# Optimization experiments

Hardware: AMD Instinct MI355X
Metric: run time of the kernel (lower is better)

Reference implementation:

```python
import jax, jax.numpy as jnp
import numpy as np

B = 1024      # jets per batch
P = 150       # TOTAL_PARTICLES per jet
N = B * P     # total nodes
DEG = 16      # avg degree
E = N * DEG
H = 256       # GNN_HIDDEN_DIM
K = 6         # GNN_K
NC = 10       # NUM_CLUSTERS
IN = 3


def setup_inputs() -> dict:
    key = jax.random.key(0)
    ks = jax.random.split(key, 16)
    x = jax.random.normal(ks[0], (N, IN), jnp.float32)
    # kNN-like within-jet edges: each node sends to DEG random nodes of its own jet
    src = jnp.repeat(jnp.arange(N, dtype=jnp.int32), DEG)
    tgt = (src // P) * P + jax.random.randint(ks[1], (E,), 0, P, dtype=jnp.int32)
    edge_index = jnp.stack([src, tgt])  # [2, E]
    batch = jnp.arange(N, dtype=jnp.int32) // P  # sorted graph ids, exactly P per graph
    inp = dict(x=x, edge_index=edge_index, batch=batch)
    dims = [(IN, H), (H, H), (H, H), (H, H)]
    for i, (di, do) in enumerate(dims):
        s = 1.0 / np.sqrt(di)
        inp[f"W{i+1}"] = jax.random.uniform(ks[2 + i], (K, di, do), jnp.float32, -s, s)
        inp[f"b{i+1}"] = jnp.zeros((do,), jnp.float32)
    for i in range(3):
        inp[f"g{i+1}"] = jnp.ones((H,), jnp.float32)
        inp[f"be{i+1}"] = jnp.zeros((H,), jnp.float32)
    inp["centers"] = jax.random.normal(ks[10], (NC, 2), jnp.float32) * 0.2
    inp["log_temp"] = jnp.float32(2.0)
    return inp


def _lap_weights(src, tgt, n):
    # PyG ChebConv norm with lambda_max=2, sym normalization, self-loops removed:
    # scaled Laplacian L_hat = -D^{-1/2} A D^{-1/2} (zero diagonal)
    w = (src != tgt).astype(jnp.float32)          # remove self-loops
    deg = jax.ops.segment_sum(w, src, num_segments=n)
    dis = jnp.where(deg > 0, 1.0 / jnp.sqrt(deg), 0.0)
    return -(dis[src] * w * dis[tgt])             # [E]


def _cheb(x, W, b, src, tgt, lw, n):
    # Chebyshev recurrence: T0=x, T1=Lx, Tk=2L T_{k-1} - T_{k-2}
    prop = lambda h: jax.ops.segment_sum(lw[:, None] * h[src], tgt, num_segments=n)
    Tx0 = x
    out = Tx0 @ W[0]
    Tx1 = prop(Tx0)
    out = out + Tx1 @ W[1]
    for k in range(2, W.shape[0]):
        Tx2 = 2.0 * prop(Tx1) - Tx0
        out = out + Tx2 @ W[k]
        Tx0, Tx1 = Tx1, Tx2
    return out + b


def _bn(h, g, b):
    # BatchNorm1d, training-mode batch statistics (biased var), eps=1e-5
    m = h.mean(0)
    v = h.var(0)
    return (h - m) * jax.lax.rsqrt(v + 1e-5) * g + b


def reference(x, edge_index, batch, W1, b1, W2, b2, W3, b3, W4, b4,
              g1, be1, g2, be2, g3, be3, centers, log_temp):
    n = x.shape[0]
    src, tgt = edge_index[0], edge_index[1]
    lw = _lap_weights(src, tgt, n)
    lrelu = lambda h: jax.nn.leaky_relu(h, 0.01)
    h = lrelu(_bn(_cheb(x, W1, b1, src, tgt, lw, n), g1, be1))
    h = lrelu(_bn(_cheb(h, W2, b2, src, tgt, lw, n), g2, be2))
    h = lrelu(_bn(_cheb(h, W3, b3, src, tgt, lw, n), g3, be3))
    h = _cheb(h, W4, b4, src, tgt, lw, n)
    h = h / jnp.maximum(jnp.linalg.norm(h, axis=1, keepdims=True), 1e-12)  # F.normalize
    # to_dense_batch: batch is sorted with exactly P nodes per graph -> pure reshape,
    # node_mask is all True
    dense_h = h.reshape(B, P, -1)          # [B, P, H]
    dense_c = x[:, :2].reshape(B, P, 2)    # (eta, phi)
    dist = ((dense_c[:, :, None, :] - centers) ** 2).sum(-1)   # [B, P, NC]
    T = jnp.exp(jnp.clip(log_temp, -2.0, 3.0))
    assignment = jax.nn.softmax(-T * dist, axis=-1)            # mask is all-true
    pooled = jnp.einsum('bnk,bnd->bkd', assignment, dense_h)   # [B, NC, H]
    pooled = pooled / (assignment.sum(1)[:, :, None] + 1e-8)
    return pooled.reshape(B, -1)  # [B, NC*H]
```

## Files before the change

kernel.cpp:

```cpp
#include <hip/hip_runtime.h>
#include <cstdio>

#define NODES 153600
#define PJ 150
#define NJETS 1024
#define DEG 16
#define NEDGE (NODES*DEG)
#define HD 256
#define NCL 10

#define LSTR 192
#define TNS  64

typedef unsigned short u16;
typedef _Float16 f16;
typedef f16 f16x8 __attribute__((ext_vector_type(8)));
typedef u16 u16x8 __attribute__((ext_vector_type(8)));
typedef u16 u16x4 __attribute__((ext_vector_type(4)));
typedef float f32x4 __attribute__((ext_vector_type(4)));

__device__ inline float h2f(u16 u) { union { u16 s; f16 h; } v; v.s = u; return (float)v.h; }
__device__ inline u16 f2h(float f) { union { u16 s; f16 h; } v; v.h = (f16)f; return v.s; }
__device__ inline int swz(int seg, int key) { return (seg & ~7) | ((seg & 7) ^ (key & 7)); }

__global__ void k_diag(float* out, float code) {
  if (blockIdx.x == 0 && threadIdx.x == 0) out[0] = code;
}


__global__ __launch_bounds__(256) void k_discounts(const int* __restrict__ tgt,
                                                   int* __restrict__ counts,
                                                   float* __restrict__ dis) {
  int i = blockIdx.x*256 + threadIdx.x;
  if (i < NEDGE) atomicAdd(&counts[tgt[i]], 1);
  if (i < NODES) {
    int cnt = 0;
#pragma unroll
    for (int j = 0; j < DEG; ++j) cnt += (tgt[i*DEG + j] != i) ? 1 : 0;
    dis[i] = (cnt > 0) ? rsqrtf((float)cnt) : 0.f;
  }
}

__global__ __launch_bounds__(256) void k_scan(const int* __restrict__ counts, int* __restrict__ rowptr, int* __restrict__ cursor) {
  int j = blockIdx.x*256 + threadIdx.x;
  if (j >= NJETS) return;
  int run = j*PJ*DEG;
  for (int l = 0; l < PJ; ++l) {
    int idx = j*PJ + l;
    int cnt = counts[idx];
    rowptr[idx] = run;
    cursor[idx] = run;
    run += cnt;
  }
  if (j == 0) rowptr[NODES] = NEDGE;
}

__global__ __launch_bounds__(256) void k_fill(const int* __restrict__ src_, const int* __restrict__ tgt_,
                                              const float* __restrict__ dis, int* __restrict__ cursor,
                                              unsigned char* __restrict__ ccol, float* __restrict__ cw) {
  int e = blockIdx.x*256 + threadIdx.x;
  if (e >= NEDGE) return;
  int s = src_[e], t = tgt_[e];
  int pos = atomicAdd(&cursor[t], 1);
  ccol[pos] = (unsigned char)(s % PJ);
  cw[pos] = (s != t) ? -(dis[s]*dis[t]) : 0.f;
}

__global__ __launch_bounds__(256) void k_prepW(const float* __restrict__ Wa, const float* __restrict__ Wb,
                                               const float* __restrict__ Wc, u16* __restrict__ WT,
                                               float* __restrict__ stats ,
                                               float* __restrict__ rn) {
  int i = blockIdx.x*256 + threadIdx.x;
  if (i < 3*256*1536) {
    int layer = i / (256*1536);
    int rem = i - layer*(256*1536);
    int cout = rem / 1536, k = rem - cout*1536;
    int term = k >> 8, cin = k & 255;
    const float* W = (layer == 0) ? Wa : (layer == 1) ? Wb : Wc;
    WT[i] = f2h(W[(size_t)term*65536 + cin*256 + cout]);
  }
  if (i < 3*2*HD) stats[i] = 0.f;
  if (i < NODES) rn[i] = 0.f;
}

__global__ __launch_bounds__(512) void k_l1(const float* __restrict__ x,
                                            const int* __restrict__ rowptr,
                                            const unsigned char* __restrict__ ccol,
                                            const float* __restrict__ cw,
                                            const float* __restrict__ W1,
                                            const float* __restrict__ b1,
                                            float* __restrict__ stats,
                                            u16* __restrict__ outc) {
  __shared__ float Ta[450], Tb[450];
  __shared__ float Tall_s[PJ*18];
  __shared__ float wl[18*256];
  __shared__ float cw_s[PJ*DEG];
  __shared__ u16  col_s[PJ*DEG];
  __shared__ int  rp_s[PJ+1];
  int j = blockIdx.x, tid = threadIdx.x;
  int jb = j*PJ, e0 = jb*DEG;
  for (int i = tid; i < 18*256; i += 512) wl[i] = W1[i];
  for (int i = tid; i < PJ*DEG; i += 512) { cw_s[i] = cw[e0+i]; col_s[i] = (u16)ccol[e0+i]; }
  for (int i = tid; i < PJ+1; i += 512) rp_s[i] = rowptr[jb+i] - e0;
  if (tid < 450) Ta[tid] = x[(size_t)jb*3 + tid];
  __syncthreads();
  int r = tid/3, c = tid - r*3;
  float* cur = Ta; float* oth = Tb;
  if (tid < 450) Tall_s[r*18 + c] = cur[tid];
  for (int t = 1; t < 6; ++t) {
    if (tid < 450) {
      int es = rp_s[r], ee = rp_s[r+1];
      float acc = 0.f;
      for (int e = es; e < ee; ++e) acc += cw_s[e]*cur[(int)col_s[e]*3 + c];
      float v = (t == 1) ? acc : 2.f*acc - oth[tid];
      oth[tid] = v;
      Tall_s[r*18 + t*3 + c] = v;
    }
    __syncthreads();
    float* tmp = cur; cur = oth; oth = tmp;
  }
  int cc = tid & 255, rhalf = tid >> 8;
  float bc = b1[cc];
  float s = 0.f, s2 = 0.f;
  int r0 = rhalf*75;
  for (int rr = r0; rr < r0 + 75; ++rr) {
    float acc = 0.f;
#pragma unroll
    for (int i = 0; i < 18; ++i) acc += Tall_s[rr*18 + i] * wl[i*256 + cc];
    outc[(size_t)(jb+rr)*HD + cc] = f2h(acc);
    float vb = acc + bc;
    s += vb; s2 += vb*vb;
  }
  atomicAdd(&stats[cc], s);
  atomicAdd(&stats[HD + cc], s2);
}

template<int OMODE>
__global__ __launch_bounds__(1024, 4) void k_cheb(const u16* __restrict__ IN,
                                                  const u16* __restrict__ WTu,
                                                  const int* __restrict__ rowptr,
                                                  const unsigned char* __restrict__ ccol,
                                                  const float* __restrict__ cw,
                                                  const float* __restrict__ statsPrev,
                                                  const float* __restrict__ gP,
                                                  const float* __restrict__ beP,
                                                  const float* __restrict__ bP,
                                                  const float* __restrict__ bCur,
                                                  float* __restrict__ statsCur,
                                                  float* __restrict__ rn,
                                                  u16* __restrict__ OUTp) {
  __shared__ u16 Ls[160*LSTR];
  __shared__ u16 Tn[2][160*TNS];
  __shared__ u16 Tt[2][64*LSTR];
  __shared__ float bnA[HD], bnB[HD];
  int j = blockIdx.x, tid = threadIdx.x;
  int jb = j*PJ;
  int lane = tid & 63, wid = tid >> 6;
  int wm = wid >> 3, wn = wid & 7;
  int lr = lane & 15, lg = lane >> 4;
  int ph = wn >> 2, cs = wn & 3;
  int cown = cs*16 + lr;
  int key   = lr & 7;
  int segA0 = ((lg    ) ^ key) * 8;
  int segA1 = ((lg + 4) ^ key) * 8;
  int pOff[5] = { segA0, segA1, 64 + segA0, 64 + segA1, 128 + segA0 };
  int ep0 = ((cown >> 3) ^ ((lg & 1)*4 + 0)) * 8 + (cown & 7);
  int ep1 = ((cown >> 3) ^ ((lg & 1)*4 + 1)) * 8 + (cown & 7);
  int ep2 = ((cown >> 3) ^ ((lg & 1)*4 + 2)) * 8 + (cown & 7);
  int ep3 = ((cown >> 3) ^ ((lg & 1)*4 + 3)) * 8 + (cown & 7);
  int cownL = cown * LSTR;
  const f16* WT = (const f16*)WTu;
  const f16* wtb = WT + (size_t)(wn*32 + lr)*1536 + lg*8;

  if (tid < HD) {
    const float invN = 1.f/(float)NODES;
    float m = statsPrev[tid]*invN;
    float var = statsPrev[HD+tid]*invN - m*m;
    float A = rsqrtf(var + 1e-5f) * gP[tid];
    bnA[tid] = A;
    bnB[tid] = (bP[tid] - m)*A + beP[tid];
  }
  {
    u16x8 z = {0,0,0,0,0,0,0,0};
    for (int i = tid; i < 3840; i += 1024) *(u16x8*)&Ls[i*8] = z;
    for (int i = tid; i < 160; i += 1024) {
      int h = i >= 80 ? 1 : 0;
      int rem = i - h*80;
      int row = 150 + (rem >> 3), seg = rem & 7;
      *(u16x8*)&Tn[h][row*TNS + seg*8] = z;
    }
  }
  __syncthreads();
  if (tid < PJ) {
    int es = rowptr[jb + tid], ee = rowptr[jb + tid + 1];
    for (int e = es; e < ee; ++e) {
      int c = (int)ccol[e];
      int a = tid*LSTR + swz(c >> 3, tid)*8 + (c & 7);
      Ls[a] = f2h(h2f(Ls[a]) + 2.f*cw[e]);
    }
  }
  f32x4 acc[5][2];
#pragma unroll
  for (int a = 0; a < 5; ++a)
#pragma unroll
    for (int b = 0; b < 2; ++b) acc[a][b] = (f32x4)0.f;

  u16x4 tc0, tc1, tc2, tc3, tc4, tp0, tp1, tp2, tp3, tp4;

  for (int qp = 0; qp < 2; ++qp) {
    __syncthreads();
    for (int i = tid; i < 2400; i += 1024) {
      int h = (i >= 1200) ? 1 : 0;
      int rem = i - h*1200;
      int row = rem >> 3, seg = rem & 7;
      int c0 = (qp*2+h)*64 + seg*8;
      u16x8 v = *(const u16x8*)&IN[(size_t)(jb+row)*HD + c0];
      u16x8 o;
#pragma unroll
      for (int u = 0; u < 8; ++u) {
        float f = h2f(v[u])*bnA[c0+u] + bnB[c0+u];
        o[u] = f2h((f > 0.f) ? f : 0.01f*f);
      }
      *(u16x8*)&Tn[h][row*TNS + (seg ^ (row & 7))*8] = o;
    }
    __syncthreads();
    for (int i = tid; i < 2560; i += 1024) {
      int h = (i >= 1280) ? 1 : 0;
      int rem = i - h*1280;
      int c = rem & 63, m = rem >> 6;
      u16x8 v;
#pragma unroll
      for (int u = 0; u < 8; ++u) {
        int r = m*8 + u;
        v[u] = Tn[h][r*TNS + ((c >> 3) ^ (r & 7))*8 + (c & 7)];
      }
      *(u16x8*)&Tt[h][c*LSTR + swz(m, c)*8] = v;
    }
#define TINIT(MF, TC, TP) { int r0 = wm*80 + MF*16 + lg*4; u16x4 t; \
    t[0] = Tn[ph][(r0+0)*TNS + ep0]; t[1] = Tn[ph][(r0+1)*TNS + ep1]; \
    t[2] = Tn[ph][(r0+2)*TNS + ep2]; t[3] = Tn[ph][(r0+3)*TNS + ep3]; \
    TC = t; TP = t; }
    TINIT(0, tc0, tp0) TINIT(1, tc1, tp1) TINIT(2, tc2, tp2) TINIT(3, tc3, tp3) TINIT(4, tc4, tp4)
#undef TINIT
    __syncthreads();
#pragma unroll 1
    for (int t = 0; t < 6; ++t) {
#pragma unroll
      for (int h = 0; h < 2; ++h) {
        int kbase = t*256 + (qp*2+h)*64;
#pragma unroll
        for (int ks = 0; ks < 64; ks += 32) {
          int segA = (ks == 0) ? segA0 : segA1;
          f16x8 a[5], bv[2];
#pragma unroll
          for (int nf = 0; nf < 2; ++nf)
            bv[nf] = *(const f16x8*)&wtb[nf*24576 + kbase + ks];
#pragma unroll
          for (int mf = 0; mf < 5; ++mf) {
            int row = wm*80 + mf*16 + lr;
            a[mf] = *(const f16x8*)&Tn[h][row*TNS + segA];
          }
#pragma unroll
          for (int nf = 0; nf < 2; ++nf)
#pragma unroll
            for (int mf = 0; mf < 5; ++mf)
              acc[mf][nf] = __builtin_amdgcn_mfma_f32_16x16x32_f16(a[mf], bv[nf], acc[mf][nf], 0, 0, 0);
        }
      }
      if (t < 5) {
        f32x4 pacc[5];
#pragma unroll
        for (int mf = 0; mf < 5; ++mf) pacc[mf] = (f32x4)0.f;
#pragma unroll
        for (int ks = 0; ks < 5; ++ks) {
          f16x8 b = *(const f16x8*)&Tt[ph][cownL + pOff[ks]];
#pragma unroll
          for (int mf = 0; mf < 5; ++mf) {
            int row = wm*80 + mf*16 + lr;
            f16x8 a = *(const f16x8*)&Ls[row*LSTR + pOff[ks]];
            pacc[mf] = __builtin_amdgcn_mfma_f32_16x16x32_f16(a, b, pacc[mf], 0, 0, 0);
          }
        }
        __syncthreads();
#define TEPI(MF, TC, TP) { int r0 = wm*80 + MF*16 + lg*4; u16x4 o; \
        { float v0_ = (t == 0) ? 0.5f*pacc[MF][0] : pacc[MF][0] - h2f(TP[0]); o[0] = f2h(v0_); } \
        { float v1_ = (t == 0) ? 0.5f*pacc[MF][1] : pacc[MF][1] - h2f(TP[1]); o[1] = f2h(v1_); } \
        { float v2_ = (t == 0) ? 0.5f*pacc[MF][2] : pacc[MF][2] - h2f(TP[2]); o[2] = f2h(v2_); } \
        { float v3_ = (t == 0) ? 0.5f*pacc[MF][3] : pacc[MF][3] - h2f(TP[3]); o[3] = f2h(v3_); } \
        Tn[ph][(r0+0)*TNS + ep0] = o[0]; Tn[ph][(r0+1)*TNS + ep1] = o[1]; \
        Tn[ph][(r0+2)*TNS + ep2] = o[2]; Tn[ph][(r0+3)*TNS + ep3] = o[3]; \
        int sgT = wm*10 + MF*2 + (lg >> 1); \
        int segT = (sgT & ~7) | ((sgT & 7) ^ key); \
        *(u16x4*)&Tt[ph][cownL + segT*8 + (lg & 1)*4] = o; \
        TP = TC; TC = o; }
        TEPI(0, tc0, tp0) TEPI(1, tc1, tp1) TEPI(2, tc2, tp2) TEPI(3, tc3, tp3) TEPI(4, tc4, tp4)
#undef TEPI
        __syncthreads();
      }
    }
  }
  if (OMODE == 0) {
#pragma unroll
    for (int nf = 0; nf < 2; ++nf) {
      int col = wn*32 + nf*16 + lr;
      float bc = bCur[col];
      float s = 0.f, s2 = 0.f;
#pragma unroll
      for (int mf = 0; mf < 5; ++mf) {
        int row = wm*80 + mf*16 + lg*4;
#pragma unroll
        for (int e = 0; e < 4; ++e) {
          int r = row + e;
          if (r < PJ) {
            float v = acc[mf][nf][e];
            OUTp[(size_t)(jb+r)*HD + col] = f2h(v);
            float vb = v + bc;
            s += vb; s2 += vb*vb;
          }
        }
      }
      s  += __shfl_xor(s, 16, 64);  s  += __shfl_xor(s, 32, 64);
      s2 += __shfl_xor(s2, 16, 64); s2 += __shfl_xor(s2, 32, 64);
      if (lg == 0) {
        atomicAdd(&statsCur[col], s);
        atomicAdd(&statsCur[HD + col], s2);
      }
    }
  } else {
    float bc[2];
#pragma unroll
    for (int nf = 0; nf < 2; ++nf) bc[nf] = bCur[wn*32 + nf*16 + lr];
#pragma unroll
    for (int mf = 0; mf < 5; ++mf) {
      int row = wm*80 + mf*16 + lg*4;
#pragma unroll
      for (int e = 0; e < 4; ++e) {
        int r = row + e;
        float srow = 0.f;
        if (r < PJ) {
#pragma unroll
          for (int nf = 0; nf < 2; ++nf) {
            int col = wn*32 + nf*16 + lr;
            float v = acc[mf][nf][e];
            OUTp[(size_t)(jb+r)*HD + col] = f2h(v);
            float vb = v + bc[nf];
            srow += vb*vb;
          }
        }
        srow += __shfl_xor(srow, 1, 64);
        srow += __shfl_xor(srow, 2, 64);
        srow += __shfl_xor(srow, 4, 64);
        srow += __shfl_xor(srow, 8, 64);
        if (lr == 0 && r < PJ) atomicAdd(&rn[jb + r], srow);
      }
    }
  }
}


__global__ __launch_bounds__(256) void k_pool(const u16* __restrict__ h, const float* __restrict__ rn,
                                              const float* __restrict__ bias, const float* __restrict__ x,
                                              const float* __restrict__ centers, const float* __restrict__ log_temp,
                                              float* __restrict__ out) {
  __shared__ float a_s[PJ][NCL];
  __shared__ float colsum[NCL];
  __shared__ float inv_s[PJ];
  int j = blockIdx.x;
  int tid = threadIdx.x;
  float T = expf(fminf(fmaxf(log_temp[0], -2.f), 3.f));
  if (tid < PJ) {
    int g = j*PJ + tid;
    inv_s[tid] = 1.f / fmaxf(sqrtf(rn[g]), 1e-12f);
    float eta = x[(size_t)g*3], phi = x[(size_t)g*3 + 1];
    float d[NCL];
    float dmin = 1e30f;
#pragma unroll
    for (int k = 0; k < NCL; ++k) {
      float dx = eta - centers[2*k], dy = phi - centers[2*k+1];
      d[k] = dx*dx + dy*dy;
      dmin = fminf(dmin, d[k]);
    }
    float s = 0.f, ek[NCL];
#pragma unroll
    for (int k = 0; k < NCL; ++k) { ek[k] = expf(-T*(d[k]-dmin)); s += ek[k]; }
    float invs = 1.f/s;
#pragma unroll
    for (int k = 0; k < NCL; ++k) a_s[tid][k] = ek[k]*invs;
  }
  __syncthreads();
  if (tid < NCL) {
    float s = 0.f;
    for (int n = 0; n < PJ; ++n) s += a_s[n][tid];
    colsum[tid] = s;
  }
  __syncthreads();
  int c = tid;
  float bc = bias[c];
  float acc[NCL] = {};
  for (int n = 0; n < PJ; ++n) {
    float hv = (h2f(h[(size_t)(j*PJ + n)*HD + c]) + bc) * inv_s[n];
#pragma unroll
    for (int k = 0; k < NCL; ++k) acc[k] += a_s[n][k]*hv;
  }
#pragma unroll
  for (int k = 0; k < NCL; ++k)
    out[(size_t)j*(NCL*HD) + k*HD + c] = acc[k] / (colsum[k] + 1e-8f);
}


extern "C" void kernel_launch(void* const* d_in, const int* in_sizes, int n_in,
                              void* d_out, int out_size, void* d_ws, size_t ws_size,
                              hipStream_t stream) {
  (void)in_sizes; (void)n_in; (void)out_size;
  const float* x   = (const float*)d_in[0];
  const int*   ei  = (const int*)d_in[1];
  const int*   srcA = ei;
  const int*   tgtA = ei + NEDGE;
  const float* W1  = (const float*)d_in[3];
  const float* b1  = (const float*)d_in[4];
  const float* W2  = (const float*)d_in[5];
  const float* b2  = (const float*)d_in[6];
  const float* W3  = (const float*)d_in[7];
  const float* b3  = (const float*)d_in[8];
  const float* W4  = (const float*)d_in[9];
  const float* b4  = (const float*)d_in[10];
  const float* g1  = (const float*)d_in[11];
  const float* be1 = (const float*)d_in[12];
  const float* g2  = (const float*)d_in[13];
  const float* be2 = (const float*)d_in[14];
  const float* g3  = (const float*)d_in[15];
  const float* be3 = (const float*)d_in[16];
  const float* centers  = (const float*)d_in[17];
  const float* log_temp = (const float*)d_in[18];
  float* out = (float*)d_out;

  auto rb = [](size_t b) { return (b + 255) & ~(size_t)255; };
  size_t need = 2*rb((size_t)NODES*HD*2)
              + rb((size_t)3*256*1536*2)
              + 3*rb((size_t)NODES*4)
              + rb((size_t)(NODES+1)*4)
              + rb((size_t)NEDGE)
              + rb((size_t)NEDGE*4)
              + rb((size_t)3*2*HD*4)
              + rb((size_t)NODES*4);
  fprintf(stderr, "[kernel_launch] ws_size=%zu need=%zu\n", ws_size, need);
  if (d_ws == nullptr || ws_size < need) {
    float code = 1.0e6f + (float)(ws_size >> 20);
    k_diag<<<1, 1, 0, stream>>>(out, code);
    return;
  }

  char* wp = (char*)d_ws;
  auto alloc = [&](size_t b) -> void* {
    void* p = (void*)wp;
    wp += (b + 255) & ~(size_t)255;
    return p;
  };
  u16*   OUTA = (u16*)alloc((size_t)NODES*HD*2);
  u16*   OUTB = (u16*)alloc((size_t)NODES*HD*2);
  u16*   Wcat = (u16*)alloc((size_t)3*256*1536*2);
  float* dis  = (float*)alloc((size_t)NODES*4);
  int*   counts = (int*)alloc((size_t)NODES*4);
  int*   cursor = (int*)alloc((size_t)NODES*4);
  int*   rowptr = (int*)alloc((size_t)(NODES+1)*4);
  unsigned char* ccol = (unsigned char*)alloc((size_t)NEDGE);
  float* cw     = (float*)alloc((size_t)NEDGE*4);
  float* stats  = (float*)alloc((size_t)3*2*HD*4);
  float* rn     = (float*)alloc((size_t)NODES*4);
  float* s0 = stats, *s1 = stats + 512, *s2 = stats + 1024;

  hipMemsetAsync(counts, 0, (size_t)NODES*4, stream);
  k_discounts<<<(NEDGE+255)/256, 256, 0, stream>>>(tgtA, counts, dis);
  k_scan<<<(NJETS+255)/256, 256, 0, stream>>>(counts, rowptr, cursor);
  k_fill<<<(NEDGE+255)/256, 256, 0, stream>>>(srcA, tgtA, dis, cursor, ccol, cw);

  k_prepW<<<(3*256*1536+255)/256, 256, 0, stream>>>(W2, W3, W4, Wcat, stats, rn);

  k_l1<<<NJETS, 512, 0, stream>>>(x, rowptr, ccol, cw, W1, b1, s0, OUTA);

  k_cheb<0><<<NJETS, 1024, 0, stream>>>(OUTA, Wcat,            rowptr, ccol, cw, s0, g1, be1, b1, b2, s1, rn, OUTB);
  k_cheb<0><<<NJETS, 1024, 0, stream>>>(OUTB, Wcat + 393216,   rowptr, ccol, cw, s1, g2, be2, b2, b3, s2, rn, OUTA);
  k_cheb<1><<<NJETS, 1024, 0, stream>>>(OUTA, Wcat + 2*393216, rowptr, ccol, cw, s2, g3, be3, b3, b4, s2, rn, OUTB);

  k_pool<<<NJETS, 256, 0, stream>>>(OUTB, rn, b4, x, centers, log_temp, out);
}
```

Before: 1.273 ms.

## Stage Chebyshev output through shared memory for coalesced stores and hoist weight loads

Merges the separate shared buffers into one pool so the output tile can be staged in shared memory after the GEMM. The global write then becomes 16-byte coalesced row stores instead of scattered 2-byte per-lane writes. The weight fragments for each recurrence step are also all loaded up front, so global weight reads are issued together ahead of the MFMAs. This costs two extra block barriers, a shared-memory round trip, and more live registers.

```diff
diff --git a/kernel.cpp b/kernel.cpp
--- a/kernel.cpp
+++ b/kernel.cpp
@@ -11,6 +11,7 @@
 
 #define LSTR 192
 #define TNS  64
+#define OSTR 264
 
 typedef unsigned short u16;
 typedef _Float16 f16;
@@ -149,10 +150,13 @@
                                                   float* __restrict__ statsCur,
                                                   float* __restrict__ rn,
                                                   u16* __restrict__ OUTp) {
-  __shared__ u16 Ls[160*LSTR];
-  __shared__ u16 Tn[2][160*TNS];
-  __shared__ u16 Tt[2][64*LSTR];
+  __shared__ u16 SM[75776];
   __shared__ float bnA[HD], bnB[HD];
+  u16* Ls  = SM;
+  u16* Tn0 = SM + 30720;
+  u16* Tn1 = SM + 40960;
+  u16* Tt0 = SM + 51200;
+  u16* Tt1 = SM + 63488;
   int j = blockIdx.x, tid = threadIdx.x;
   int jb = j*PJ;
   int lane = tid & 63, wid = tid >> 6;
@@ -160,6 +164,8 @@
   int lr = lane & 15, lg = lane >> 4;
   int ph = wn >> 2, cs = wn & 3;
   int cown = cs*16 + lr;
+  u16* Tnp = ph ? Tn1 : Tn0;
+  u16* Ttp = ph ? Tt1 : Tt0;
   int key   = lr & 7;
   int segA0 = ((lg    ) ^ key) * 8;
   int segA1 = ((lg + 4) ^ key) * 8;
@@ -187,7 +193,8 @@
       int h = i >= 80 ? 1 : 0;
       int rem = i - h*80;
       int row = 150 + (rem >> 3), seg = rem & 7;
-      *(u16x8*)&Tn[h][row*TNS + seg*8] = z;
+      u16* TnH = h ? Tn1 : Tn0;
+      *(u16x8*)&TnH[row*TNS + seg*8] = z;
     }
   }
   __syncthreads();
@@ -221,59 +228,61 @@
         float f = h2f(v[u])*bnA[c0+u] + bnB[c0+u];
         o[u] = f2h((f > 0.f) ? f : 0.01f*f);
       }
-      *(u16x8*)&Tn[h][row*TNS + (seg ^ (row & 7))*8] = o;
+      u16* TnH = h ? Tn1 : Tn0;
+      *(u16x8*)&TnH[row*TNS + (seg ^ (row & 7))*8] = o;
     }
     __syncthreads();
     for (int i = tid; i < 2560; i += 1024) {
       int h = (i >= 1280) ? 1 : 0;
       int rem = i - h*1280;
       int c = rem & 63, m = rem >> 6;
+      u16* TnH = h ? Tn1 : Tn0;
+      u16* TtH = h ? Tt1 : Tt0;
       u16x8 v;
 #pragma unroll
       for (int u = 0; u < 8; ++u) {
         int r = m*8 + u;
-        v[u] = Tn[h][r*TNS + ((c >> 3) ^ (r & 7))*8 + (c & 7)];
+        v[u] = TnH[r*TNS + ((c >> 3) ^ (r & 7))*8 + (c & 7)];
       }
-      *(u16x8*)&Tt[h][c*LSTR + swz(m, c)*8] = v;
+      *(u16x8*)&TtH[c*LSTR + swz(m, c)*8] = v;
     }
 #define TINIT(MF, TC, TP) { int r0 = wm*80 + MF*16 + lg*4; u16x4 t; \
-    t[0] = Tn[ph][(r0+0)*TNS + ep0]; t[1] = Tn[ph][(r0+1)*TNS + ep1]; \
-    t[2] = Tn[ph][(r0+2)*TNS + ep2]; t[3] = Tn[ph][(r0+3)*TNS + ep3]; \
+    t[0] = Tnp[(r0+0)*TNS + ep0]; t[1] = Tnp[(r0+1)*TNS + ep1]; \
+    t[2] = Tnp[(r0+2)*TNS + ep2]; t[3] = Tnp[(r0+3)*TNS + ep3]; \
     TC = t; TP = t; }
     TINIT(0, tc0, tp0) TINIT(1, tc1, tp1) TINIT(2, tc2, tp2) TINIT(3, tc3, tp3) TINIT(4, tc4, tp4)
 #undef TINIT
     __syncthreads();
 #pragma unroll 1
     for (int t = 0; t < 6; ++t) {
-#pragma unroll
-      for (int h = 0; h < 2; ++h) {
-        int kbase = t*256 + (qp*2+h)*64;
-#pragma unroll
-        for (int ks = 0; ks < 64; ks += 32) {
-          int segA = (ks == 0) ? segA0 : segA1;
-          f16x8 a[5], bv[2];
-#pragma unroll
-          for (int nf = 0; nf < 2; ++nf)
-            bv[nf] = *(const f16x8*)&wtb[nf*24576 + kbase + ks];
-#pragma unroll
-          for (int mf = 0; mf < 5; ++mf) {
-            int row = wm*80 + mf*16 + lr;
-            a[mf] = *(const f16x8*)&Tn[h][row*TNS + segA];
-          }
-#pragma unroll
-          for (int nf = 0; nf < 2; ++nf)
-#pragma unroll
-            for (int mf = 0; mf < 5; ++mf)
-              acc[mf][nf] = __builtin_amdgcn_mfma_f32_16x16x32_f16(a[mf], bv[nf], acc[mf][nf], 0, 0, 0);
-        }
-      }
+      int kb0 = t*256 + qp*128;
+      f16x8 w000 = *(const f16x8*)&wtb[        kb0      ];
+      f16x8 w001 = *(const f16x8*)&wtb[24576 + kb0      ];
+      f16x8 w010 = *(const f16x8*)&wtb[        kb0 + 32 ];
+      f16x8 w011 = *(const f16x8*)&wtb[24576 + kb0 + 32 ];
+      f16x8 w100 = *(const f16x8*)&wtb[        kb0 + 64 ];
+      f16x8 w101 = *(const f16x8*)&wtb[24576 + kb0 + 64 ];
+      f16x8 w110 = *(const f16x8*)&wtb[        kb0 + 96 ];
+      f16x8 w111 = *(const f16x8*)&wtb[24576 + kb0 + 96 ];
+#define WGEMM(TNH, SEGA, BV0, BV1) { f16x8 a_[5]; \
+      _Pragma("unroll") for (int mf = 0; mf < 5; ++mf) { \
+        int row = wm*80 + mf*16 + lr; \
+        a_[mf] = *(const f16x8*)&TNH[row*TNS + SEGA]; } \
+      _Pragma("unroll") for (int mf = 0; mf < 5; ++mf) { \
+        acc[mf][0] = __builtin_amdgcn_mfma_f32_16x16x32_f16(a_[mf], BV0, acc[mf][0], 0, 0, 0); \
+        acc[mf][1] = __builtin_amdgcn_mfma_f32_16x16x32_f16(a_[mf], BV1, acc[mf][1], 0, 0, 0); } }
+      WGEMM(Tn0, segA0, w000, w001)
+      WGEMM(Tn0, segA1, w010, w011)
+      WGEMM(Tn1, segA0, w100, w101)
+      WGEMM(Tn1, segA1, w110, w111)
+#undef WGEMM
       if (t < 5) {
         f32x4 pacc[5];
 #pragma unroll
         for (int mf = 0; mf < 5; ++mf) pacc[mf] = (f32x4)0.f;
 #pragma unroll
         for (int ks = 0; ks < 5; ++ks) {
-          f16x8 b = *(const f16x8*)&Tt[ph][cownL + pOff[ks]];
+          f16x8 b = *(const f16x8*)&Ttp[cownL + pOff[ks]];
 #pragma unroll
           for (int mf = 0; mf < 5; ++mf) {
             int row = wm*80 + mf*16 + lr;
@@ -287,11 +296,11 @@
         { float v1_ = (t == 0) ? 0.5f*pacc[MF][1] : pacc[MF][1] - h2f(TP[1]); o[1] = f2h(v1_); } \
         { float v2_ = (t == 0) ? 0.5f*pacc[MF][2] : pacc[MF][2] - h2f(TP[2]); o[2] = f2h(v2_); } \
         { float v3_ = (t == 0) ? 0.5f*pacc[MF][3] : pacc[MF][3] - h2f(TP[3]); o[3] = f2h(v3_); } \
-        Tn[ph][(r0+0)*TNS + ep0] = o[0]; Tn[ph][(r0+1)*TNS + ep1] = o[1]; \
-        Tn[ph][(r0+2)*TNS + ep2] = o[2]; Tn[ph][(r0+3)*TNS + ep3] = o[3]; \
+        Tnp[(r0+0)*TNS + ep0] = o[0]; Tnp[(r0+1)*TNS + ep1] = o[1]; \
+        Tnp[(r0+2)*TNS + ep2] = o[2]; Tnp[(r0+3)*TNS + ep3] = o[3]; \
         int sgT = wm*10 + MF*2 + (lg >> 1); \
         int segT = (sgT & ~7) | ((sgT & 7) ^ key); \
-        *(u16x4*)&Tt[ph][cownL + segT*8 + (lg & 1)*4] = o; \
+        *(u16x4*)&Ttp[cownL + segT*8 + (lg & 1)*4] = o; \
         TP = TC; TC = o; }
         TEPI(0, tc0, tp0) TEPI(1, tc1, tp1) TEPI(2, tc2, tp2) TEPI(3, tc3, tp3) TEPI(4, tc4, tp4)
 #undef TEPI
@@ -299,6 +308,8 @@
       }
     }
   }
+  __syncthreads();
+  u16* OutS = SM;
   if (OMODE == 0) {
 #pragma unroll
     for (int nf = 0; nf < 2; ++nf) {
@@ -313,7 +324,7 @@
           int r = row + e;
           if (r < PJ) {
             float v = acc[mf][nf][e];
-            OUTp[(size_t)(jb+r)*HD + col] = f2h(v);
+            OutS[r*OSTR + col] = f2h(v);
             float vb = v + bc;
             s += vb; s2 += vb*vb;
           }
@@ -342,7 +353,7 @@
           for (int nf = 0; nf < 2; ++nf) {
             int col = wn*32 + nf*16 + lr;
             float v = acc[mf][nf][e];
-            OUTp[(size_t)(jb+r)*HD + col] = f2h(v);
+            OutS[r*OSTR + col] = f2h(v);
             float vb = v + bc[nf];
             srow += vb*vb;
           }
@@ -354,6 +365,11 @@
         if (lr == 0 && r < PJ) atomicAdd(&rn[jb + r], srow);
       }
     }
+  }
+  __syncthreads();
+  for (int i = tid; i < 4800; i += 1024) {
+    int row = i >> 5, seg = i & 31;
+    *(u16x8*)&OUTp[(size_t)(jb+row)*HD + seg*8] = *(const u16x8*)&OutS[row*OSTR + seg*8];
   }
 }
 
```

Result: slower. 1.668 ms (+31.0%).
